# Kernel optimization log

Measured on AMD Instinct MI355X. Metric: run time of the kernel, lower is better.

## Reference

```python
import jax, jax.numpy as jnp
import numpy as np

N_BASIS = 128   # n_atom_basis F
N_INT   = 3     # n_interactions
N_RBF   = 20
CUTOFF  = 5.0
MAX_Z   = 100
EPS     = 1e-8
N_ATOMS = 25000
N_EDGES = 200000


def setup_inputs() -> dict:
    key = jax.random.key(0)
    ks = jax.random.split(key, 16)
    F = N_BASIS
    s = 0.02
    z     = jax.random.randint(ks[0], (N_ATOMS,), 1, MAX_Z)
    pos   = jax.random.uniform(ks[1], (N_ATOMS, 3), dtype=jnp.float32) * 2.0  # small box -> inside cutoff
    idx_i = jax.random.randint(ks[2], (N_EDGES,), 0, N_ATOMS)
    idx_j = jax.random.randint(ks[3], (N_EDGES,), 0, N_ATOMS)
    emb   = jax.random.normal(ks[4], (MAX_Z, F), dtype=jnp.float32) * s
    fW    = jax.random.normal(ks[5], (N_RBF, 3 * F * N_INT), dtype=jnp.float32) * s
    fb    = jnp.zeros((3 * F * N_INT,), jnp.float32)
    iW1   = jax.random.normal(ks[6], (N_INT, F, F), dtype=jnp.float32) * s
    ib1   = jnp.zeros((N_INT, F), jnp.float32)
    iW2   = jax.random.normal(ks[7], (N_INT, F, 3 * F), dtype=jnp.float32) * s
    ib2   = jnp.zeros((N_INT, 3 * F), jnp.float32)
    mWmix = jax.random.normal(ks[8], (N_INT, F, 2 * F), dtype=jnp.float32) * s
    mW1   = jax.random.normal(ks[9], (N_INT, 2 * F, F), dtype=jnp.float32) * s
    mb1   = jnp.zeros((N_INT, F), jnp.float32)
    mW2   = jax.random.normal(ks[10], (N_INT, F, 3 * F), dtype=jnp.float32) * s
    mb2   = jnp.zeros((N_INT, 3 * F), jnp.float32)
    return dict(z=z, pos=pos, idx_i=idx_i, idx_j=idx_j, emb=emb, fW=fW, fb=fb,
                iW1=iW1, ib1=ib1, iW2=iW2, ib2=ib2,
                mWmix=mWmix, mW1=mW1, mb1=mb1, mW2=mW2, mb2=mb2)


def reference(z, pos, idx_i, idx_j, emb, fW, fb, iW1, ib1, iW2, ib2,
              mWmix, mW1, mb1, mW2, mb2):
    F = N_BASIS
    n_atoms = z.shape[0]
    # geometry
    r_ij = pos[idx_j] - pos[idx_i]                                  # [E,3]
    r_ij = jnp.where(jnp.abs(r_ij) < 1e-6, 1e-6, r_ij)
    d_ij = jnp.linalg.norm(r_ij, axis=1, keepdims=True)             # [E,1]
    dir_ij = r_ij / d_ij                                            # [E,3]
    # Gaussian radial basis
    offsets = jnp.linspace(0.0, CUTOFF, N_RBF)
    width = offsets[1] - offsets[0]
    coeff = -0.5 / (width * width)
    phi = jnp.exp(coeff * (d_ij[..., None] - offsets) ** 2)         # [E,1,n_rbf]
    # cosine cutoff
    fcut = 0.5 * (jnp.cos(jnp.pi * d_ij / CUTOFF) + 1.0) * (d_ij < CUTOFF)  # [E,1]
    filters = (phi @ fW + fb) * fcut[..., None]                     # [E,1,3F*I]
    filter_list = jnp.split(filters, N_INT, axis=-1)                # each [E,1,3F]
    # initial atom features
    q = emb[z][:, None, :]                                          # [N,1,F]
    mu = jnp.zeros((n_atoms, 3, F), q.dtype)                        # [N,3,F]
    for t in range(N_INT):
        # --- interaction (gather - filter-multiply - scatter-add) ---
        x = jax.nn.silu(q @ iW1[t] + ib1[t]) @ iW2[t] + ib2[t]      # [N,1,3F]
        xj = x[idx_j]                                               # [E,1,3F]
        muj = mu[idx_j]                                             # [E,3,F]
        x = filter_list[t] * xj                                     # [E,1,3F]
        dq, dmuR, dmumu = jnp.split(x, 3, axis=-1)                  # [E,1,F] each
        dq = jax.ops.segment_sum(dq, idx_i, num_segments=n_atoms)   # [N,1,F]
        dmu = dmuR * dir_ij[..., None] + dmumu * muj                # [E,3,F]
        dmu = jax.ops.segment_sum(dmu, idx_i, num_segments=n_atoms) # [N,3,F]
        q = q + dq
        mu = mu + dmu
        # --- mixing (intra-atomic) ---
        mu_mix = mu @ mWmix[t]                                      # [N,3,2F]
        mu_V, mu_W = jnp.split(mu_mix, 2, axis=-1)                  # [N,3,F]
        mu_Vn = jnp.sqrt(jnp.sum(mu_V ** 2, axis=-2, keepdims=True) + EPS)  # [N,1,F]
        ctx = jnp.concatenate([q, mu_Vn], axis=-1)                  # [N,1,2F]
        x = jax.nn.silu(ctx @ mW1[t] + mb1[t]) @ mW2[t] + mb2[t]    # [N,1,3F]
        dq_intra, dmu_intra, dqmu_intra = jnp.split(x, 3, axis=-1)
        dmu_intra = dmu_intra * mu_W                                # [N,3,F]
        dqmu_intra = dqmu_intra * jnp.sum(mu_V * mu_W, axis=1, keepdims=True)
        q = q + dq_intra + dqmu_intra
        mu = mu + dmu_intra
    return q.squeeze(1), mu
```

## Files before the change

kernel.cpp:

```cpp
#include <hip/hip_runtime.h>
#include <hip/hip_bf16.h>

#define F 128
#define F3 384
#define NRBF 20
#define NITER 3

typedef __hip_bfloat16 bf16;
typedef __bf16 bfrag __attribute__((ext_vector_type(8)));
typedef float f32x4 __attribute__((ext_vector_type(4)));

__device__ __forceinline__ float b2f(bf16 v) { return __bfloat162float(v); }
__device__ __forceinline__ bf16 f2b(float v) { return __float2bfloat16(v); }
__device__ __forceinline__ bfrag ldb(const bf16* p) { return *(const bfrag*)p; }
__device__ __forceinline__ bfrag ldsb(const __bf16* p) { return *(const bfrag*)p; }
__device__ __forceinline__ bfrag cvtf(const float* p) {
    bfrag r;
#pragma unroll
    for (int j = 0; j < 8; ++j) r[j] = (__bf16)p[j];
    return r;
}

__global__ void detect_kernel(const unsigned short* __restrict__ raw, int n_u16,
                              int* __restrict__ flag) {
    int i = blockIdx.x * blockDim.x + threadIdx.x;
    int bad = 0;
    for (int k = i; k < n_u16; k += blockDim.x * gridDim.x) {
        unsigned e = (raw[k] >> 7) & 0xFFu;
        if (e >= 140u) bad = 1;
    }
    if (bad) atomicOr(flag, 1);
}

__global__ void cvt_dual_kernel(const void* __restrict__ src, float* __restrict__ dst,
                                int n, const int* __restrict__ flag) {
    int i = blockIdx.x * blockDim.x + threadIdx.x;
    if (i >= n) return;
    if (*flag) dst[i] = ((const float*)src)[i];
    else       dst[i] = b2f(((const bf16*)src)[i]);
}

__global__ void transpose_bf16_kernel(const float* __restrict__ src, bf16* __restrict__ dst,
                                      int K, int Nn, int total) {
    int i = blockIdx.x * blockDim.x + threadIdx.x;
    if (i >= total) return;
    int slice = K * Nn;
    int t = i / slice, j = i - t * slice;
    int n = j / K, k = j - n * K;
    dst[i] = f2b(src[t * slice + k * Nn + n]);
}

__global__ void geom_kernel(const float* __restrict__ pos, const int* __restrict__ ii,
                            const int* __restrict__ jj, float* __restrict__ dirv,
                            float* __restrict__ fcutv, bf16* __restrict__ phifc, int E) {
    int e = blockIdx.x * blockDim.x + threadIdx.x;
    if (e >= E) return;
    int i = ii[e], j = jj[e];
    float r[3];
#pragma unroll
    for (int d = 0; d < 3; ++d) {
        float v = pos[j * 3 + d] - pos[i * 3 + d];
        if (fabsf(v) < 1e-6f) v = 1e-6f;
        r[d] = v;
    }
    float dd = sqrtf(r[0] * r[0] + r[1] * r[1] + r[2] * r[2]);
    float inv = 1.0f / dd;
    dirv[e * 3 + 0] = r[0] * inv;
    dirv[e * 3 + 1] = r[1] * inv;
    dirv[e * 3 + 2] = r[2] * inv;
    const float CUT = 5.0f;
    const float PI = 3.14159265358979323846f;
    float fc = (dd < CUT) ? 0.5f * (cosf(PI * dd / CUT) + 1.0f) : 0.0f;
    fcutv[e] = fc;
    const float width = CUT / (NRBF - 1);
    const float coeff = -0.5f / (width * width);
#pragma unroll
    for (int k = 0; k < NRBF; ++k) {
        float diff = dd - (float)k * width;
        phifc[e * NRBF + k] = f2b(expf(coeff * diff * diff) * fc);
    }
}

__global__ void embed_kernel(const int* __restrict__ z, const float* __restrict__ emb,
                             float* __restrict__ q, int N) {
    int idx = blockIdx.x * blockDim.x + threadIdx.x;
    if (idx >= N * F) return;
    int n = idx >> 7, f = idx & 127;
    q[idx] = emb[z[n] * F + f];
}

__global__ void count_kernel(const int* __restrict__ ii, int* __restrict__ counts, int E) {
    int e = blockIdx.x * blockDim.x + threadIdx.x;
    if (e < E) atomicAdd(&counts[ii[e]], 1);
}

__global__ void scan_kernel(const int* __restrict__ counts, int* __restrict__ offs, int N) {
    __shared__ int cum[1024];
    int t = threadIdx.x;
    int chunk = (N + 1023) >> 10;
    int b = t * chunk;
    int e = b + chunk; if (e > N) e = N;
    int s = 0;
    for (int a = b; a < e; ++a) s += counts[a];
    cum[t] = s;
    __syncthreads();
    for (int o = 1; o < 1024; o <<= 1) {
        int u = (t >= o) ? cum[t - o] : 0;
        __syncthreads();
        cum[t] += u;
        __syncthreads();
    }
    int run = cum[t] - s;
    for (int a = b; a < e; ++a) { offs[a] = run; run += counts[a]; }
    if (t == 1023) offs[N] = cum[1023];
}

__global__ void fill_kernel(const int* __restrict__ ii, const int* __restrict__ offs,
                            int* __restrict__ cursor, int* __restrict__ elist, int E) {
    int e = blockIdx.x * blockDim.x + threadIdx.x;
    if (e >= E) return;
    int i = ii[e];
    int p = atomicAdd(&cursor[i], 1);
    elist[offs[i] + p] = e;
}

__global__ __launch_bounds__(256) void atom_x_mfma(
    const float* __restrict__ q, const bf16* __restrict__ W1T, const float* __restrict__ b1,
    const bf16* __restrict__ W2T, const float* __restrict__ b2, bf16* __restrict__ x, int N) {
    __shared__ __bf16 H[32][136];
    int tid = threadIdx.x;
    int w = tid >> 6, l = tid & 63;
    int lm = l & 15, q4 = l >> 4;
    int i0 = blockIdx.x * 32;
    f32x4 acc[2][2] = {};
    int r0 = min(i0 + lm, N - 1);
    int r1 = min(i0 + 16 + lm, N - 1);
    for (int kt = 0; kt < 4; ++kt) {
        int ko = kt * 32 + q4 * 8;
        bfrag a0 = cvtf(q + (size_t)r0 * F + ko);
        bfrag a1 = cvtf(q + (size_t)r1 * F + ko);
        bfrag b0 = ldb(W1T + (size_t)(w * 32 + lm) * F + ko);
        bfrag b1f = ldb(W1T + (size_t)(w * 32 + 16 + lm) * F + ko);
        acc[0][0] = __builtin_amdgcn_mfma_f32_16x16x32_bf16(a0, b0, acc[0][0], 0, 0, 0);
        acc[1][0] = __builtin_amdgcn_mfma_f32_16x16x32_bf16(a1, b0, acc[1][0], 0, 0, 0);
        acc[0][1] = __builtin_amdgcn_mfma_f32_16x16x32_bf16(a0, b1f, acc[0][1], 0, 0, 0);
        acc[1][1] = __builtin_amdgcn_mfma_f32_16x16x32_bf16(a1, b1f, acc[1][1], 0, 0, 0);
    }
#pragma unroll
    for (int nt = 0; nt < 2; ++nt) {
        int col = w * 32 + nt * 16 + lm;
        float bb = b1[col];
#pragma unroll
        for (int mt = 0; mt < 2; ++mt)
#pragma unroll
            for (int r = 0; r < 4; ++r) {
                float v = acc[mt][nt][r] + bb;
                H[mt * 16 + q4 * 4 + r][col] = (__bf16)(v / (1.0f + expf(-v)));
            }
    }
    __syncthreads();
#pragma unroll
    for (int j = 0; j < 6; ++j) {
        int n0 = w * 96 + j * 16;
        f32x4 c0 = {}, c1 = {};
        const bf16* bp = W2T + (size_t)(n0 + lm) * F;
        for (int kt = 0; kt < 4; ++kt) {
            int ko = kt * 32 + q4 * 8;
            bfrag a0 = ldsb(&H[lm][ko]);
            bfrag a1 = ldsb(&H[16 + lm][ko]);
            bfrag bf = ldb(bp + ko);
            c0 = __builtin_amdgcn_mfma_f32_16x16x32_bf16(a0, bf, c0, 0, 0, 0);
            c1 = __builtin_amdgcn_mfma_f32_16x16x32_bf16(a1, bf, c1, 0, 0, 0);
        }
        int col = n0 + lm;
        float bb = b2[col];
#pragma unroll
        for (int r = 0; r < 4; ++r) {
            int row0 = i0 + q4 * 4 + r;
            int row1 = row0 + 16;
            if (row0 < N) x[(size_t)row0 * F3 + col] = f2b(c0[r] + bb);
            if (row1 < N) x[(size_t)row1 * F3 + col] = f2b(c1[r] + bb);
        }
    }
}

__global__ void edge_gather_kernel(float* __restrict__ q, const bf16* __restrict__ mu_in,
                                   const bf16* __restrict__ x, const float* __restrict__ dirv,
                                   const float* __restrict__ fcutv, const bf16* __restrict__ phifc,
                                   const float* __restrict__ fW_f, const float* __restrict__ fb_f,
                                   int t, const int* __restrict__ offs, const int* __restrict__ elist,
                                   const int* __restrict__ jj, bf16* __restrict__ mu_out, int N) {
    int i = blockIdx.x;
    int f = threadIdx.x;
    const float* fWt = fW_f + t * F3;
    const float* fbt = fb_f + t * F3;
    float w0[NRBF], w1[NRBF], w2[NRBF];
#pragma unroll
    for (int k = 0; k < NRBF; ++k) {
        const float* row = fWt + k * (3 * F * NITER);
        w0[k] = row[f];
        w1[k] = row[f + 128];
        w2[k] = row[f + 256];
    }
    float fb0 = fbt[f], fb1 = fbt[f + 128], fb2 = fbt[f + 256];
    int beg = offs[i], end = offs[i + 1];
    float accq = 0.0f, am0 = 0.0f, am1 = 0.0f, am2 = 0.0f;
    for (int l = beg; l < end; ++l) {
        int e = elist[l];
        int j = jj[e];
        float fc = fcutv[e];
        float f0 = fc * fb0, f1 = fc * fb1, f2 = fc * fb2;
#pragma unroll
        for (int k = 0; k < NRBF; ++k) {
            float ph = b2f(phifc[e * NRBF + k]);
            f0 += ph * w0[k];
            f1 += ph * w1[k];
            f2 += ph * w2[k];
        }
        const bf16* xj = x + (size_t)j * F3;
        float dq = f0 * b2f(xj[f]);
        float dR = f1 * b2f(xj[f + 128]);
        float dM = f2 * b2f(xj[f + 256]);
        accq += dq;
        float d0 = dirv[e * 3 + 0], d1 = dirv[e * 3 + 1], d2 = dirv[e * 3 + 2];
        const bf16* muj = mu_in + (size_t)j * F3;
        am0 += dR * d0 + dM * b2f(muj[f]);
        am1 += dR * d1 + dM * b2f(muj[f + 128]);
        am2 += dR * d2 + dM * b2f(muj[f + 256]);
    }
    q[(size_t)i * F + f] += accq;
    mu_out[(size_t)i * F3 + f]       = f2b(b2f(mu_in[(size_t)i * F3 + f]) + am0);
    mu_out[(size_t)i * F3 + 128 + f] = f2b(b2f(mu_in[(size_t)i * F3 + 128 + f]) + am1);
    mu_out[(size_t)i * F3 + 256 + f] = f2b(b2f(mu_in[(size_t)i * F3 + 256 + f]) + am2);
}

__global__ __launch_bounds__(256) void mix_mfma(
    float* __restrict__ q, bf16* __restrict__ mu,
    const bf16* __restrict__ WmixT, const bf16* __restrict__ W1T, const float* __restrict__ b1,
    const bf16* __restrict__ W2T, const float* __restrict__ b2, int N) {
    __shared__ __bf16 MM[48][264];
    __shared__ __bf16 CT[16][264];
    __shared__ __bf16 HM[16][136];
    __shared__ __bf16 Y[16][392];
    int tid = threadIdx.x;
    int w = tid >> 6, l = tid & 63;
    int lm = l & 15, q4 = l >> 4;
    int i0 = blockIdx.x * 16;
    int rowsM = N * 3;
    {
        f32x4 acc[3][4] = {};
        int mr[3];
#pragma unroll
        for (int mt = 0; mt < 3; ++mt) mr[mt] = min(i0 * 3 + mt * 16 + lm, rowsM - 1);
        for (int kt = 0; kt < 4; ++kt) {
            int ko = kt * 32 + q4 * 8;
            bfrag a[3], b[4];
#pragma unroll
            for (int mt = 0; mt < 3; ++mt) a[mt] = ldb(mu + (size_t)mr[mt] * F + ko);
#pragma unroll
            for (int nt = 0; nt < 4; ++nt)
                b[nt] = ldb(WmixT + (size_t)(w * 64 + nt * 16 + lm) * F + ko);
#pragma unroll
            for (int mt = 0; mt < 3; ++mt)
#pragma unroll
                for (int nt = 0; nt < 4; ++nt)
                    acc[mt][nt] = __builtin_amdgcn_mfma_f32_16x16x32_bf16(a[mt], b[nt], acc[mt][nt], 0, 0, 0);
        }
#pragma unroll
        for (int mt = 0; mt < 3; ++mt)
#pragma unroll
            for (int nt = 0; nt < 4; ++nt)
#pragma unroll
                for (int r = 0; r < 4; ++r)
                    MM[mt * 16 + q4 * 4 + r][w * 64 + nt * 16 + lm] = (__bf16)acc[mt][nt][r];
    }
    __syncthreads();
    for (int idx = tid; idx < 16 * F; idx += 256) {
        int a = idx >> 7, f = idx & 127;
        int i = min(i0 + a, N - 1);
        float v0 = (float)MM[a * 3 + 0][f];
        float v1 = (float)MM[a * 3 + 1][f];
        float v2 = (float)MM[a * 3 + 2][f];
        CT[a][f] = (__bf16)q[(size_t)i * F + f];
        CT[a][F + f] = (__bf16)sqrtf(v0 * v0 + v1 * v1 + v2 * v2 + 1e-8f);
    }
    __syncthreads();
    {
        f32x4 c[2] = {};
        for (int kt = 0; kt < 8; ++kt) {
            int ko = kt * 32 + q4 * 8;
            bfrag a = ldsb(&CT[lm][ko]);
#pragma unroll
            for (int nt = 0; nt < 2; ++nt) {
                bfrag b = ldb(W1T + (size_t)(w * 32 + nt * 16 + lm) * 256 + ko);
                c[nt] = __builtin_amdgcn_mfma_f32_16x16x32_bf16(a, b, c[nt], 0, 0, 0);
            }
        }
#pragma unroll
        for (int nt = 0; nt < 2; ++nt) {
            int col = w * 32 + nt * 16 + lm;
            float bb = b1[col];
#pragma unroll
            for (int r = 0; r < 4; ++r) {
                float v = c[nt][r] + bb;
                HM[q4 * 4 + r][col] = (__bf16)(v / (1.0f + expf(-v)));
            }
        }
    }
    __syncthreads();
#pragma unroll
    for (int j = 0; j < 6; ++j) {
        int n0 = w * 96 + j * 16;
        f32x4 c = {};
        const bf16* bp = W2T + (size_t)(n0 + lm) * F;
        for (int kt = 0; kt < 4; ++kt) {
            int ko = kt * 32 + q4 * 8;
            bfrag a = ldsb(&HM[lm][ko]);
            bfrag b = ldb(bp + ko);
            c = __builtin_amdgcn_mfma_f32_16x16x32_bf16(a, b, c, 0, 0, 0);
        }
        int col = n0 + lm;
        float bb = b2[col];
#pragma unroll
        for (int r = 0; r < 4; ++r)
            Y[q4 * 4 + r][col] = (__bf16)(c[r] + bb);
    }
    __syncthreads();
    for (int idx = tid; idx < 16 * F; idx += 256) {
        int a = idx >> 7, f = idx & 127;
        int i = i0 + a;
        if (i >= N) continue;
        float V0 = (float)MM[a * 3 + 0][f], W0 = (float)MM[a * 3 + 0][F + f];
        float V1 = (float)MM[a * 3 + 1][f], W1v = (float)MM[a * 3 + 1][F + f];
        float V2 = (float)MM[a * 3 + 2][f], W2v = (float)MM[a * 3 + 2][F + f];
        float s = V0 * W0 + V1 * W1v + V2 * W2v;
        float yq = (float)Y[a][f], ym = (float)Y[a][F + f], ys = (float)Y[a][2 * F + f];
        q[(size_t)i * F + f] += yq + ys * s;
        size_t mb = (size_t)i * F3 + f;
        mu[mb]       = f2b(b2f(mu[mb]) + ym * W0);
        mu[mb + 128] = f2b(b2f(mu[mb + 128]) + ym * W1v);
        mu[mb + 256] = f2b(b2f(mu[mb + 256]) + ym * W2v);
    }
}

__global__ void out_kernel(const float* __restrict__ q, const bf16* __restrict__ mu,
                           void* __restrict__ out, int N, const int* __restrict__ flag) {
    int idx = blockIdx.x * blockDim.x + threadIdx.x;
    int nq = N * F;
    int tot = nq + N * F3;
    if (idx >= tot) return;
    float v = (idx < nq) ? q[idx] : b2f(mu[idx - nq]);
    if (*flag) ((float*)out)[idx] = v;
    else       ((bf16*)out)[idx] = f2b(v);
}

extern "C" void kernel_launch(void* const* d_in, const int* in_sizes, int n_in,
                              void* d_out, int out_size, void* d_ws, size_t ws_size,
                              hipStream_t stream) {
    const int* z = (const int*)d_in[0];
    const int* idx_i = (const int*)d_in[2];
    const int* idx_j = (const int*)d_in[3];

    int N = in_sizes[0];
    int E = in_sizes[2];

    char* base = (char*)d_ws;
    size_t off = 0;
    auto alloc = [&](size_t bytes) -> void* {
        void* p = base + off;
        off += (bytes + 255) & ~(size_t)255;
        return p;
    };

    int* flag = (int*)alloc(4);
    float* pos_f = (float*)alloc((size_t)in_sizes[1] * 4);
    float* emb_f = (float*)alloc((size_t)in_sizes[4] * 4);
    float* fW_f = (float*)alloc((size_t)in_sizes[5] * 4);
    float* fb_f = (float*)alloc((size_t)in_sizes[6] * 4);
    float* iW1_f = (float*)alloc((size_t)in_sizes[7] * 4);
    float* ib1_f = (float*)alloc((size_t)in_sizes[8] * 4);
    float* iW2_f = (float*)alloc((size_t)in_sizes[9] * 4);
    float* ib2_f = (float*)alloc((size_t)in_sizes[10] * 4);
    float* mWmix_f = (float*)alloc((size_t)in_sizes[11] * 4);
    float* mW1_f = (float*)alloc((size_t)in_sizes[12] * 4);
    float* mb1_f = (float*)alloc((size_t)in_sizes[13] * 4);
    float* mW2_f = (float*)alloc((size_t)in_sizes[14] * 4);
    float* mb2_f = (float*)alloc((size_t)in_sizes[15] * 4);
    bf16* iW1T = (bf16*)alloc((size_t)NITER * F * F * 2);
    bf16* iW2T = (bf16*)alloc((size_t)NITER * F3 * F * 2);
    bf16* mWmixT = (bf16*)alloc((size_t)NITER * 2 * F * F * 2);
    bf16* mW1T = (bf16*)alloc((size_t)NITER * F * 2 * F * 2);
    bf16* mW2T = (bf16*)alloc((size_t)NITER * F3 * F * 2);
    float* q = (float*)alloc((size_t)N * F * 4);
    bf16* mua = (bf16*)alloc((size_t)N * F3 * 2);
    bf16* mub = (bf16*)alloc((size_t)N * F3 * 2);
    bf16* xbuf = (bf16*)alloc((size_t)N * F3 * 2);
    float* dirv = (float*)alloc((size_t)E * 3 * 4);
    float* fcutv = (float*)alloc((size_t)E * 4);
    bf16* phifc = (bf16*)alloc((size_t)E * NRBF * 2);
    int* counts = (int*)alloc((size_t)N * 4);
    int* offs = (int*)alloc((size_t)(N + 1) * 4);
    int* elist = (int*)alloc((size_t)E * 4);

    hipMemsetAsync(flag, 0, 4, stream);
    detect_kernel<<<64, 256, 0, stream>>>((const unsigned short*)d_in[1], in_sizes[1], flag);

    auto cvt = [&](int idx, float* dst) {
        int n = in_sizes[idx];
        cvt_dual_kernel<<<(n + 255) / 256, 256, 0, stream>>>(d_in[idx], dst, n, flag);
    };
    cvt(1, pos_f);
    cvt(4, emb_f);
    cvt(5, fW_f);  cvt(6, fb_f);
    cvt(7, iW1_f); cvt(8, ib1_f);
    cvt(9, iW2_f); cvt(10, ib2_f);
    cvt(11, mWmix_f);
    cvt(12, mW1_f); cvt(13, mb1_f);
    cvt(14, mW2_f); cvt(15, mb2_f);

    auto tpose = [&](const float* src, bf16* dst, int K, int Nn) {
        int total = NITER * K * Nn;
        transpose_bf16_kernel<<<(total + 255) / 256, 256, 0, stream>>>(src, dst, K, Nn, total);
    };
    tpose(iW1_f, iW1T, F, F);
    tpose(iW2_f, iW2T, F, F3);
    tpose(mWmix_f, mWmixT, F, 2 * F);
    tpose(mW1_f, mW1T, 2 * F, F);
    tpose(mW2_f, mW2T, F, F3);

    geom_kernel<<<(E + 255) / 256, 256, 0, stream>>>(pos_f, idx_i, idx_j, dirv, fcutv, phifc, E);
    embed_kernel<<<(N * F + 255) / 256, 256, 0, stream>>>(z, emb_f, q, N);
    hipMemsetAsync(mua, 0, (size_t)N * F3 * 2, stream);

    hipMemsetAsync(counts, 0, (size_t)N * 4, stream);
    count_kernel<<<(E + 255) / 256, 256, 0, stream>>>(idx_i, counts, E);
    scan_kernel<<<1, 1024, 0, stream>>>(counts, offs, N);
    hipMemsetAsync(counts, 0, (size_t)N * 4, stream);
    fill_kernel<<<(E + 255) / 256, 256, 0, stream>>>(idx_i, offs, counts, elist, E);

    bf16* muin = mua;
    bf16* muout = mub;
    for (int t = 0; t < NITER; ++t) {
        atom_x_mfma<<<(N + 31) / 32, 256, 0, stream>>>(q, iW1T + (size_t)t * F * F, ib1_f + t * F,
                                                       iW2T + (size_t)t * F3 * F, ib2_f + t * F3,
                                                       xbuf, N);
        edge_gather_kernel<<<N, 128, 0, stream>>>(q, muin, xbuf, dirv, fcutv, phifc, fW_f, fb_f,
                                                  t, offs, elist, idx_j, muout, N);
        mix_mfma<<<(N + 15) / 16, 256, 0, stream>>>(q, muout, mWmixT + (size_t)t * 2 * F * F,
                                                    mW1T + (size_t)t * F * 2 * F, mb1_f + t * F,
                                                    mW2T + (size_t)t * F3 * F, mb2_f + t * F3, N);
        bf16* tm = muin; muin = muout; muout = tm;
    }

    int tot = N * (F + F3);
    out_kernel<<<(tot + 255) / 256, 256, 0, stream>>>(q, muin, d_out, N, flag);
}
```

Measured before the change: 890.8 us.

## Compute edge filters with MFMA and store edge data in CSR order

Edge geometry outputs (rbf*fcut padded to 32 with the cutoff as a bias column, direction, neighbor index) are now written directly in destination-sorted order, so the edge loop no longer goes through elist. The per-edge filter projection (20 rbf + bias to 384 channels) now runs as bf16 MFMA on chunks of 16 edges per atom instead of scalar FMAs with per-thread weight registers. Work is split across 384 threads so that separate waves handle the q, radial-mu and mu-mu terms, with a shared-memory reduction at the end. The cost is extra synchronisation per 16-edge chunk and poor MFMA utilisation for atoms with few edges (about 8 on average).

```diff
diff --git a/kernel.cpp b/kernel.cpp
--- a/kernel.cpp
+++ b/kernel.cpp
@@ -50,12 +50,24 @@
     dst[i] = f2b(src[t * slice + k * Nn + n]);
 }
 
+__global__ void fwt_kernel(const float* __restrict__ fW, const float* __restrict__ fb,
+                           bf16* __restrict__ dst, int total) {
+    int idx = blockIdx.x * blockDim.x + threadIdx.x;
+    if (idx >= total) return;
+    int k = idx & 31, rest = idx >> 5;
+    int n = rest % F3, t = rest / F3;
+    float v = (k < NRBF) ? fW[k * (F3 * NITER) + t * F3 + n]
+                         : (k == NRBF ? fb[t * F3 + n] : 0.0f);
+    dst[idx] = f2b(v);
+}
+
 __global__ void geom_kernel(const float* __restrict__ pos, const int* __restrict__ ii,
-                            const int* __restrict__ jj, float* __restrict__ dirv,
-                            float* __restrict__ fcutv, bf16* __restrict__ phifc, int E) {
+                            const int* __restrict__ jj, const int* __restrict__ rank,
+                            bf16* __restrict__ phifc2, float* __restrict__ dir2,
+                            int* __restrict__ jj2, int E) {
     int e = blockIdx.x * blockDim.x + threadIdx.x;
     if (e >= E) return;
-    int i = ii[e], j = jj[e];
+    int i = ii[e], j = jj[e], l = rank[e];
     float r[3];
 #pragma unroll
     for (int d = 0; d < 3; ++d) {
@@ -65,20 +77,24 @@
     }
     float dd = sqrtf(r[0] * r[0] + r[1] * r[1] + r[2] * r[2]);
     float inv = 1.0f / dd;
-    dirv[e * 3 + 0] = r[0] * inv;
-    dirv[e * 3 + 1] = r[1] * inv;
-    dirv[e * 3 + 2] = r[2] * inv;
+    jj2[l] = j;
+#pragma unroll
+    for (int d = 0; d < 3; ++d) dir2[(size_t)l * 4 + d] = r[d] * inv;
+    dir2[(size_t)l * 4 + 3] = 0.0f;
     const float CUT = 5.0f;
     const float PI = 3.14159265358979323846f;
     float fc = (dd < CUT) ? 0.5f * (cosf(PI * dd / CUT) + 1.0f) : 0.0f;
-    fcutv[e] = fc;
     const float width = CUT / (NRBF - 1);
     const float coeff = -0.5f / (width * width);
+    bf16* pr = phifc2 + (size_t)l * 32;
 #pragma unroll
     for (int k = 0; k < NRBF; ++k) {
         float diff = dd - (float)k * width;
-        phifc[e * NRBF + k] = f2b(expf(coeff * diff * diff) * fc);
-    }
+        pr[k] = f2b(expf(coeff * diff * diff) * fc);
+    }
+    pr[NRBF] = f2b(fc);
+#pragma unroll
+    for (int k = NRBF + 1; k < 32; ++k) pr[k] = f2b(0.0f);
 }
 
 __global__ void embed_kernel(const int* __restrict__ z, const float* __restrict__ emb,
@@ -116,12 +132,12 @@
 }
 
 __global__ void fill_kernel(const int* __restrict__ ii, const int* __restrict__ offs,
-                            int* __restrict__ cursor, int* __restrict__ elist, int E) {
+                            int* __restrict__ cursor, int* __restrict__ rank, int E) {
     int e = blockIdx.x * blockDim.x + threadIdx.x;
     if (e >= E) return;
     int i = ii[e];
     int p = atomicAdd(&cursor[i], 1);
-    elist[offs[i] + p] = e;
+    rank[e] = offs[i] + p;
 }
 
 __global__ __launch_bounds__(256) void atom_x_mfma(
@@ -184,54 +200,93 @@
     }
 }
 
-__global__ void edge_gather_kernel(float* __restrict__ q, const bf16* __restrict__ mu_in,
-                                   const bf16* __restrict__ x, const float* __restrict__ dirv,
-                                   const float* __restrict__ fcutv, const bf16* __restrict__ phifc,
-                                   const float* __restrict__ fW_f, const float* __restrict__ fb_f,
-                                   int t, const int* __restrict__ offs, const int* __restrict__ elist,
-                                   const int* __restrict__ jj, bf16* __restrict__ mu_out, int N) {
+__global__ __launch_bounds__(384) void edge_gather_mfma(
+    float* __restrict__ q, const bf16* __restrict__ mu_in, const bf16* __restrict__ x,
+    const bf16* __restrict__ phifc2, const float* __restrict__ dir2,
+    const int* __restrict__ jj2, const bf16* __restrict__ fWT,
+    const int* __restrict__ offs, bf16* __restrict__ mu_out, int N) {
+    __shared__ float filtS[16][393];
+    __shared__ float dirS[16][4];
+    __shared__ int jjS[16];
+    __shared__ float Rs[128][3];
+    __shared__ float Ms[128][3];
     int i = blockIdx.x;
-    int f = threadIdx.x;
-    const float* fWt = fW_f + t * F3;
-    const float* fbt = fb_f + t * F3;
-    float w0[NRBF], w1[NRBF], w2[NRBF];
-#pragma unroll
-    for (int k = 0; k < NRBF; ++k) {
-        const float* row = fWt + k * (3 * F * NITER);
-        w0[k] = row[f];
-        w1[k] = row[f + 128];
-        w2[k] = row[f + 256];
-    }
-    float fb0 = fbt[f], fb1 = fbt[f + 128], fb2 = fbt[f + 256];
+    int tid = threadIdx.x;
+    int w = tid >> 6, l = tid & 63;
+    int lm = l & 15, q4 = l >> 4;
     int beg = offs[i], end = offs[i + 1];
-    float accq = 0.0f, am0 = 0.0f, am1 = 0.0f, am2 = 0.0f;
-    for (int l = beg; l < end; ++l) {
-        int e = elist[l];
-        int j = jj[e];
-        float fc = fcutv[e];
-        float f0 = fc * fb0, f1 = fc * fb1, f2 = fc * fb2;
-#pragma unroll
-        for (int k = 0; k < NRBF; ++k) {
-            float ph = b2f(phifc[e * NRBF + k]);
-            f0 += ph * w0[k];
-            f1 += ph * w1[k];
-            f2 += ph * w2[k];
-        }
-        const bf16* xj = x + (size_t)j * F3;
-        float dq = f0 * b2f(xj[f]);
-        float dR = f1 * b2f(xj[f + 128]);
-        float dM = f2 * b2f(xj[f + 256]);
-        accq += dq;
-        float d0 = dirv[e * 3 + 0], d1 = dirv[e * 3 + 1], d2 = dirv[e * 3 + 2];
-        const bf16* muj = mu_in + (size_t)j * F3;
-        am0 += dR * d0 + dM * b2f(muj[f]);
-        am1 += dR * d1 + dM * b2f(muj[f + 128]);
-        am2 += dR * d2 + dM * b2f(muj[f + 256]);
-    }
-    q[(size_t)i * F + f] += accq;
-    mu_out[(size_t)i * F3 + f]       = f2b(b2f(mu_in[(size_t)i * F3 + f]) + am0);
-    mu_out[(size_t)i * F3 + 128 + f] = f2b(b2f(mu_in[(size_t)i * F3 + 128 + f]) + am1);
-    mu_out[(size_t)i * F3 + 256 + f] = f2b(b2f(mu_in[(size_t)i * F3 + 256 + f]) + am2);
+    bfrag Bf[4];
+#pragma unroll
+    for (int j = 0; j < 4; ++j)
+        Bf[j] = ldb(fWT + (size_t)(w * 64 + j * 16 + lm) * 32 + q4 * 8);
+    float dq = 0.f;
+    float amR0 = 0.f, amR1 = 0.f, amR2 = 0.f;
+    float amM0 = 0.f, amM1 = 0.f, amM2 = 0.f;
+    for (int c0 = beg; c0 < end; c0 += 16) {
+        int cnt = min(16, end - c0);
+        if (tid < 16) jjS[tid] = (tid < cnt) ? jj2[c0 + tid] : 0;
+        else if (tid >= 64 && tid < 128) {
+            int idx = tid - 64;
+            int le = idx >> 2, d = idx & 3;
+            dirS[le][d] = (le < cnt) ? dir2[(size_t)(c0 + le) * 4 + d] : 0.f;
+        }
+        bfrag A = ldb(phifc2 + (size_t)(c0 + lm) * 32 + q4 * 8);
+        f32x4 C[4] = {};
+#pragma unroll
+        for (int j = 0; j < 4; ++j)
+            C[j] = __builtin_amdgcn_mfma_f32_16x16x32_bf16(A, Bf[j], C[j], 0, 0, 0);
+#pragma unroll
+        for (int j = 0; j < 4; ++j) {
+            int col = w * 64 + j * 16 + lm;
+#pragma unroll
+            for (int r = 0; r < 4; ++r)
+                filtS[q4 * 4 + r][col] = C[j][r];
+        }
+        __syncthreads();
+        if (w < 2) {
+            int f = tid;
+            for (int le = 0; le < cnt; ++le) {
+                int j = jjS[le];
+                dq += filtS[le][f] * b2f(x[(size_t)j * F3 + f]);
+            }
+        } else if (w < 4) {
+            int g = tid - 128;
+            for (int le = 0; le < cnt; ++le) {
+                int j = jjS[le];
+                float dR = filtS[le][128 + g] * b2f(x[(size_t)j * F3 + 128 + g]);
+                amR0 += dR * dirS[le][0];
+                amR1 += dR * dirS[le][1];
+                amR2 += dR * dirS[le][2];
+            }
+        } else {
+            int g = tid - 256;
+            for (int le = 0; le < cnt; ++le) {
+                int j = jjS[le];
+                const bf16* mj = mu_in + (size_t)j * F3 + g;
+                float dM = filtS[le][256 + g] * b2f(x[(size_t)j * F3 + 256 + g]);
+                amM0 += dM * b2f(mj[0]);
+                amM1 += dM * b2f(mj[128]);
+                amM2 += dM * b2f(mj[256]);
+            }
+        }
+        __syncthreads();
+    }
+    if (w >= 2 && w < 4) {
+        int g = tid - 128;
+        Rs[g][0] = amR0; Rs[g][1] = amR1; Rs[g][2] = amR2;
+    } else if (w >= 4) {
+        int g = tid - 256;
+        Ms[g][0] = amM0; Ms[g][1] = amM1; Ms[g][2] = amM2;
+    }
+    __syncthreads();
+    if (tid < 128) {
+        int f = tid;
+        q[(size_t)i * F + f] += dq;
+        size_t mb = (size_t)i * F3 + f;
+#pragma unroll
+        for (int d = 0; d < 3; ++d)
+            mu_out[mb + d * 128] = f2b(b2f(mu_in[mb + d * 128]) + Rs[f][d] + Ms[f][d]);
+    }
 }
 
 __global__ __launch_bounds__(256) void mix_mfma(
@@ -391,16 +446,17 @@
     bf16* mWmixT = (bf16*)alloc((size_t)NITER * 2 * F * F * 2);
     bf16* mW1T = (bf16*)alloc((size_t)NITER * F * 2 * F * 2);
     bf16* mW2T = (bf16*)alloc((size_t)NITER * F3 * F * 2);
+    bf16* fWT = (bf16*)alloc((size_t)NITER * F3 * 32 * 2);
     float* q = (float*)alloc((size_t)N * F * 4);
     bf16* mua = (bf16*)alloc((size_t)N * F3 * 2);
     bf16* mub = (bf16*)alloc((size_t)N * F3 * 2);
     bf16* xbuf = (bf16*)alloc((size_t)N * F3 * 2);
-    float* dirv = (float*)alloc((size_t)E * 3 * 4);
-    float* fcutv = (float*)alloc((size_t)E * 4);
-    bf16* phifc = (bf16*)alloc((size_t)E * NRBF * 2);
+    bf16* phifc2 = (bf16*)alloc((size_t)(E + 16) * 32 * 2);
+    float* dir2 = (float*)alloc((size_t)(E + 16) * 4 * 4);
+    int* jj2 = (int*)alloc((size_t)(E + 16) * 4);
+    int* rank = (int*)alloc((size_t)E * 4);
     int* counts = (int*)alloc((size_t)N * 4);
     int* offs = (int*)alloc((size_t)(N + 1) * 4);
-    int* elist = (int*)alloc((size_t)E * 4);
 
     hipMemsetAsync(flag, 0, 4, stream);
     detect_kernel<<<64, 256, 0, stream>>>((const unsigned short*)d_in[1], in_sizes[1], flag);
@@ -427,16 +483,21 @@
     tpose(mWmix_f, mWmixT, F, 2 * F);
     tpose(mW1_f, mW1T, 2 * F, F);
     tpose(mW2_f, mW2T, F, F3);
-
-    geom_kernel<<<(E + 255) / 256, 256, 0, stream>>>(pos_f, idx_i, idx_j, dirv, fcutv, phifc, E);
-    embed_kernel<<<(N * F + 255) / 256, 256, 0, stream>>>(z, emb_f, q, N);
-    hipMemsetAsync(mua, 0, (size_t)N * F3 * 2, stream);
+    {
+        int total = NITER * F3 * 32;
+        fwt_kernel<<<(total + 255) / 256, 256, 0, stream>>>(fW_f, fb_f, fWT, total);
+    }
 
     hipMemsetAsync(counts, 0, (size_t)N * 4, stream);
     count_kernel<<<(E + 255) / 256, 256, 0, stream>>>(idx_i, counts, E);
     scan_kernel<<<1, 1024, 0, stream>>>(counts, offs, N);
     hipMemsetAsync(counts, 0, (size_t)N * 4, stream);
-    fill_kernel<<<(E + 255) / 256, 256, 0, stream>>>(idx_i, offs, counts, elist, E);
+    fill_kernel<<<(E + 255) / 256, 256, 0, stream>>>(idx_i, offs, counts, rank, E);
+
+    geom_kernel<<<(E + 255) / 256, 256, 0, stream>>>(pos_f, idx_i, idx_j, rank,
+                                                     phifc2, dir2, jj2, E);
+    embed_kernel<<<(N * F + 255) / 256, 256, 0, stream>>>(z, emb_f, q, N);
+    hipMemsetAsync(mua, 0, (size_t)N * F3 * 2, stream);
 
     bf16* muin = mua;
     bf16* muout = mub;
@@ -444,8 +505,8 @@
         atom_x_mfma<<<(N + 31) / 32, 256, 0, stream>>>(q, iW1T + (size_t)t * F * F, ib1_f + t * F,
                                                        iW2T + (size_t)t * F3 * F, ib2_f + t * F3,
                                                        xbuf, N);
-        edge_gather_kernel<<<N, 128, 0, stream>>>(q, muin, xbuf, dirv, fcutv, phifc, fW_f, fb_f,
-                                                  t, offs, elist, idx_j, muout, N);
+        edge_gather_mfma<<<N, 384, 0, stream>>>(q, muin, xbuf, phifc2, dir2, jj2,
+                                                fWT + (size_t)t * F3 * 32, offs, muout, N);
         mix_mfma<<<(N + 15) / 16, 256, 0, stream>>>(q, muout, mWmixT + (size_t)t * 2 * F * F,
                                                     mW1T + (size_t)t * F * 2 * F, mb1_f + t * F,
                                                     mW2T + (size_t)t * F3 * F, mb2_f + t * F3, N);
```

Result: slower. 919.2 us (+3.2%).

## Store edge geometry in CSR order and repack filter weights per feature

Applied to the files above, without the earlier changes.

The geometry kernel now runs after the CSR build and writes phi*fcut (as fp32, padded to 24 with fcut in the bias slot), directions and j indices directly at each edge's sorted rank. The gather loop then reads them contiguously instead of going through the elist indirection. Filter weights and bias are pre-transposed into a per-feature padded layout, so the bias folds into the dot product. The trade-off is more bytes per edge (fp32 instead of bf16 phi) and a scattered write in geom.

```diff
diff --git a/kernel.cpp b/kernel.cpp
--- a/kernel.cpp
+++ b/kernel.cpp
@@ -5,6 +5,7 @@
 #define F3 384
 #define NRBF 20
 #define NITER 3
+#define KP 24
 
 typedef __hip_bfloat16 bf16;
 typedef __bf16 bfrag __attribute__((ext_vector_type(8)));
@@ -50,12 +51,24 @@
     dst[i] = f2b(src[t * slice + k * Nn + n]);
 }
 
+__global__ void fwt_kernel(const float* __restrict__ fW, const float* __restrict__ fb,
+                           float* __restrict__ dst, int total) {
+    int idx = blockIdx.x * blockDim.x + threadIdx.x;
+    if (idx >= total) return;
+    int k = idx % KP, rest = idx / KP;
+    int n = rest % F3, t = rest / F3;
+    float v = (k < NRBF) ? fW[k * (F3 * NITER) + t * F3 + n]
+                         : (k == NRBF ? fb[t * F3 + n] : 0.0f);
+    dst[idx] = v;
+}
+
 __global__ void geom_kernel(const float* __restrict__ pos, const int* __restrict__ ii,
-                            const int* __restrict__ jj, float* __restrict__ dirv,
-                            float* __restrict__ fcutv, bf16* __restrict__ phifc, int E) {
+                            const int* __restrict__ jj, const int* __restrict__ rank,
+                            float* __restrict__ phifc2, float* __restrict__ dir2,
+                            int* __restrict__ jj2, int E) {
     int e = blockIdx.x * blockDim.x + threadIdx.x;
     if (e >= E) return;
-    int i = ii[e], j = jj[e];
+    int i = ii[e], j = jj[e], l = rank[e];
     float r[3];
 #pragma unroll
     for (int d = 0; d < 3; ++d) {
@@ -65,20 +78,25 @@
     }
     float dd = sqrtf(r[0] * r[0] + r[1] * r[1] + r[2] * r[2]);
     float inv = 1.0f / dd;
-    dirv[e * 3 + 0] = r[0] * inv;
-    dirv[e * 3 + 1] = r[1] * inv;
-    dirv[e * 3 + 2] = r[2] * inv;
+    jj2[l] = j;
+#pragma unroll
+    for (int d = 0; d < 3; ++d) dir2[(size_t)l * 4 + d] = r[d] * inv;
+    dir2[(size_t)l * 4 + 3] = 0.0f;
     const float CUT = 5.0f;
     const float PI = 3.14159265358979323846f;
     float fc = (dd < CUT) ? 0.5f * (cosf(PI * dd / CUT) + 1.0f) : 0.0f;
-    fcutv[e] = fc;
     const float width = CUT / (NRBF - 1);
     const float coeff = -0.5f / (width * width);
+    float* pr = phifc2 + (size_t)l * KP;
 #pragma unroll
     for (int k = 0; k < NRBF; ++k) {
         float diff = dd - (float)k * width;
-        phifc[e * NRBF + k] = f2b(expf(coeff * diff * diff) * fc);
-    }
+        pr[k] = expf(coeff * diff * diff) * fc;
+    }
+    pr[NRBF] = fc;
+    pr[NRBF + 1] = 0.0f;
+    pr[NRBF + 2] = 0.0f;
+    pr[NRBF + 3] = 0.0f;
 }
 
 __global__ void embed_kernel(const int* __restrict__ z, const float* __restrict__ emb,
@@ -116,12 +134,12 @@
 }
 
 __global__ void fill_kernel(const int* __restrict__ ii, const int* __restrict__ offs,
-                            int* __restrict__ cursor, int* __restrict__ elist, int E) {
+                            int* __restrict__ cursor, int* __restrict__ rank, int E) {
     int e = blockIdx.x * blockDim.x + threadIdx.x;
     if (e >= E) return;
     int i = ii[e];
     int p = atomicAdd(&cursor[i], 1);
-    elist[offs[i] + p] = e;
+    rank[e] = offs[i] + p;
 }
 
 __global__ __launch_bounds__(256) void atom_x_mfma(
@@ -184,54 +202,56 @@
     }
 }
 
-__global__ void edge_gather_kernel(float* __restrict__ q, const bf16* __restrict__ mu_in,
-                                   const bf16* __restrict__ x, const float* __restrict__ dirv,
-                                   const float* __restrict__ fcutv, const bf16* __restrict__ phifc,
-                                   const float* __restrict__ fW_f, const float* __restrict__ fb_f,
-                                   int t, const int* __restrict__ offs, const int* __restrict__ elist,
-                                   const int* __restrict__ jj, bf16* __restrict__ mu_out, int N) {
+__global__ __launch_bounds__(128, 2) void edge_gather_reg(
+    float* __restrict__ q, const bf16* __restrict__ mu_in, const bf16* __restrict__ x,
+    const float* __restrict__ phifc2, const float* __restrict__ dir2,
+    const int* __restrict__ jj2, const float* __restrict__ fWTf,
+    const int* __restrict__ offs, bf16* __restrict__ mu_out, int N) {
     int i = blockIdx.x;
     int f = threadIdx.x;
-    const float* fWt = fW_f + t * F3;
-    const float* fbt = fb_f + t * F3;
-    float w0[NRBF], w1[NRBF], w2[NRBF];
-#pragma unroll
-    for (int k = 0; k < NRBF; ++k) {
-        const float* row = fWt + k * (3 * F * NITER);
-        w0[k] = row[f];
-        w1[k] = row[f + 128];
-        w2[k] = row[f + 256];
-    }
-    float fb0 = fbt[f], fb1 = fbt[f + 128], fb2 = fbt[f + 256];
+    float w0[NRBF + 1], w1[NRBF + 1], w2[NRBF + 1];
+    {
+        const float* p0 = fWTf + (size_t)f * KP;
+        const float* p1 = fWTf + (size_t)(f + 128) * KP;
+        const float* p2 = fWTf + (size_t)(f + 256) * KP;
+#pragma unroll
+        for (int k = 0; k <= NRBF; ++k) {
+            w0[k] = p0[k];
+            w1[k] = p1[k];
+            w2[k] = p2[k];
+        }
+    }
     int beg = offs[i], end = offs[i + 1];
     float accq = 0.0f, am0 = 0.0f, am1 = 0.0f, am2 = 0.0f;
     for (int l = beg; l < end; ++l) {
-        int e = elist[l];
-        int j = jj[e];
-        float fc = fcutv[e];
-        float f0 = fc * fb0, f1 = fc * fb1, f2 = fc * fb2;
-#pragma unroll
-        for (int k = 0; k < NRBF; ++k) {
-            float ph = b2f(phifc[e * NRBF + k]);
+        const float* pr = phifc2 + (size_t)l * KP;
+        float f0 = 0.0f, f1 = 0.0f, f2 = 0.0f;
+#pragma unroll
+        for (int k = 0; k <= NRBF; ++k) {
+            float ph = pr[k];
             f0 += ph * w0[k];
             f1 += ph * w1[k];
             f2 += ph * w2[k];
         }
+        int j = jj2[l];
         const bf16* xj = x + (size_t)j * F3;
         float dq = f0 * b2f(xj[f]);
         float dR = f1 * b2f(xj[f + 128]);
         float dM = f2 * b2f(xj[f + 256]);
         accq += dq;
-        float d0 = dirv[e * 3 + 0], d1 = dirv[e * 3 + 1], d2 = dirv[e * 3 + 2];
+        float d0 = dir2[(size_t)l * 4 + 0];
+        float d1 = dir2[(size_t)l * 4 + 1];
+        float d2 = dir2[(size_t)l * 4 + 2];
         const bf16* muj = mu_in + (size_t)j * F3;
         am0 += dR * d0 + dM * b2f(muj[f]);
         am1 += dR * d1 + dM * b2f(muj[f + 128]);
         am2 += dR * d2 + dM * b2f(muj[f + 256]);
     }
     q[(size_t)i * F + f] += accq;
-    mu_out[(size_t)i * F3 + f]       = f2b(b2f(mu_in[(size_t)i * F3 + f]) + am0);
-    mu_out[(size_t)i * F3 + 128 + f] = f2b(b2f(mu_in[(size_t)i * F3 + 128 + f]) + am1);
-    mu_out[(size_t)i * F3 + 256 + f] = f2b(b2f(mu_in[(size_t)i * F3 + 256 + f]) + am2);
+    size_t mb = (size_t)i * F3 + f;
+    mu_out[mb]       = f2b(b2f(mu_in[mb]) + am0);
+    mu_out[mb + 128] = f2b(b2f(mu_in[mb + 128]) + am1);
+    mu_out[mb + 256] = f2b(b2f(mu_in[mb + 256]) + am2);
 }
 
 __global__ __launch_bounds__(256) void mix_mfma(
@@ -391,16 +411,17 @@
     bf16* mWmixT = (bf16*)alloc((size_t)NITER * 2 * F * F * 2);
     bf16* mW1T = (bf16*)alloc((size_t)NITER * F * 2 * F * 2);
     bf16* mW2T = (bf16*)alloc((size_t)NITER * F3 * F * 2);
+    float* fWTf = (float*)alloc((size_t)NITER * F3 * KP * 4);
     float* q = (float*)alloc((size_t)N * F * 4);
     bf16* mua = (bf16*)alloc((size_t)N * F3 * 2);
     bf16* mub = (bf16*)alloc((size_t)N * F3 * 2);
     bf16* xbuf = (bf16*)alloc((size_t)N * F3 * 2);
-    float* dirv = (float*)alloc((size_t)E * 3 * 4);
-    float* fcutv = (float*)alloc((size_t)E * 4);
-    bf16* phifc = (bf16*)alloc((size_t)E * NRBF * 2);
+    float* phifc2 = (float*)alloc((size_t)(E + 16) * KP * 4);
+    float* dir2 = (float*)alloc((size_t)(E + 16) * 4 * 4);
+    int* jj2 = (int*)alloc((size_t)(E + 16) * 4);
+    int* rank = (int*)alloc((size_t)E * 4);
     int* counts = (int*)alloc((size_t)N * 4);
     int* offs = (int*)alloc((size_t)(N + 1) * 4);
-    int* elist = (int*)alloc((size_t)E * 4);
 
     hipMemsetAsync(flag, 0, 4, stream);
     detect_kernel<<<64, 256, 0, stream>>>((const unsigned short*)d_in[1], in_sizes[1], flag);
@@ -427,16 +448,21 @@
     tpose(mWmix_f, mWmixT, F, 2 * F);
     tpose(mW1_f, mW1T, 2 * F, F);
     tpose(mW2_f, mW2T, F, F3);
-
-    geom_kernel<<<(E + 255) / 256, 256, 0, stream>>>(pos_f, idx_i, idx_j, dirv, fcutv, phifc, E);
-    embed_kernel<<<(N * F + 255) / 256, 256, 0, stream>>>(z, emb_f, q, N);
-    hipMemsetAsync(mua, 0, (size_t)N * F3 * 2, stream);
+    {
+        int total = NITER * F3 * KP;
+        fwt_kernel<<<(total + 255) / 256, 256, 0, stream>>>(fW_f, fb_f, fWTf, total);
+    }
 
     hipMemsetAsync(counts, 0, (size_t)N * 4, stream);
     count_kernel<<<(E + 255) / 256, 256, 0, stream>>>(idx_i, counts, E);
     scan_kernel<<<1, 1024, 0, stream>>>(counts, offs, N);
     hipMemsetAsync(counts, 0, (size_t)N * 4, stream);
-    fill_kernel<<<(E + 255) / 256, 256, 0, stream>>>(idx_i, offs, counts, elist, E);
+    fill_kernel<<<(E + 255) / 256, 256, 0, stream>>>(idx_i, offs, counts, rank, E);
+
+    geom_kernel<<<(E + 255) / 256, 256, 0, stream>>>(pos_f, idx_i, idx_j, rank,
+                                                     phifc2, dir2, jj2, E);
+    embed_kernel<<<(N * F + 255) / 256, 256, 0, stream>>>(z, emb_f, q, N);
+    hipMemsetAsync(mua, 0, (size_t)N * F3 * 2, stream);
 
     bf16* muin = mua;
     bf16* muout = mub;
@@ -444,8 +470,8 @@
         atom_x_mfma<<<(N + 31) / 32, 256, 0, stream>>>(q, iW1T + (size_t)t * F * F, ib1_f + t * F,
                                                        iW2T + (size_t)t * F3 * F, ib2_f + t * F3,
                                                        xbuf, N);
-        edge_gather_kernel<<<N, 128, 0, stream>>>(q, muin, xbuf, dirv, fcutv, phifc, fW_f, fb_f,
-                                                  t, offs, elist, idx_j, muout, N);
+        edge_gather_reg<<<N, 128, 0, stream>>>(q, muin, xbuf, phifc2, dir2, jj2,
+                                               fWTf + (size_t)t * F3 * KP, offs, muout, N);
         mix_mfma<<<(N + 15) / 16, 256, 0, stream>>>(q, muout, mWmixT + (size_t)t * 2 * F * F,
                                                     mW1T + (size_t)t * F * 2 * F, mb1_f + t * F,
                                                     mW2T + (size_t)t * F3 * F, mb2_f + t * F3, N);
```

Result: faster. 832.3 us (-6.6%).
